# Kernel optimization log

Measured on AMD Instinct MI355X. Metric: run time of the kernel, lower is better.

Reference implementation:

```python
import jax, jax.numpy as jnp
import numpy as np

B, F_IN, N_D, N_A, VBS, N_STEPS = 1024, 256, 64, 64, 128, 3
FO = N_D + N_A            # 128
D_CAT = 2 * F_IN          # 512
AD = F_IN                 # attention_dim = 256
GAMMA, EPSILON, BN_EPS = 1.3, 1e-15, 1e-5
SQRT_HALF = 0.7071067811865476


def _bn(x, w, b):
    # full-batch BatchNorm1d (training mode, biased var)
    m = x.mean(0)
    v = x.var(0)
    return (x - m) / jnp.sqrt(v + BN_EPS) * w + b


def _gbn(x, w, b):
    # Ghost BatchNorm: per virtual-batch statistics
    n, f = x.shape
    xr = x.reshape(n // VBS, VBS, f)
    m = xr.mean(1, keepdims=True)
    v = xr.var(1, keepdims=True)
    return (xr - m).reshape(n, f) / jnp.sqrt(v + BN_EPS).repeat(VBS, axis=0).reshape(n, f) * w + b


def _glu(x, fcw, bnw, bnb):
    h = _gbn(x @ fcw.T, bnw, bnb)
    d = h.shape[-1] // 2
    return h[:, :d] * jax.nn.sigmoid(h[:, d:])


def _feat_transformer(x, fc0, bnw0, bnb0, fc1, bnw1, bnb1):
    # independent GLU block, first=True, n_glu_independent=2
    h = _glu(x, fc0, bnw0, bnb0)
    return (h + _glu(h, fc1, bnw1, bnb1)) * SQRT_HALF


def _sparsemax(z):
    f = z.shape[-1]
    zs = -jnp.sort(-z, axis=-1)                      # descending
    k = jnp.arange(1, f + 1, dtype=z.dtype)
    zc = jnp.cumsum(zs, axis=-1)
    support = (1.0 + k * zs) > zc
    kz = jnp.sum(support, axis=-1, keepdims=True)
    tau = (jnp.take_along_axis(zc, kz - 1, axis=-1) - 1.0) / kz.astype(z.dtype)
    return jnp.maximum(z - tau, 0.0)


def _self_attn_1d(x, in_w, in_b, out_w, out_b):
    # nn.MultiheadAttention(embed_dim=1, heads=1) over the feature axis
    q = x * in_w[0] + in_b[0]
    k = x * in_w[1] + in_b[1]
    v = x * in_w[2] + in_b[2]
    attn = jax.nn.softmax(jnp.einsum('bi,bj->bij', q, k), axis=-1)  # scale 1/sqrt(1)
    y = jnp.einsum('bij,bj->bi', attn, v) * out_w + out_b
    return y, attn


def setup_inputs() -> dict:
    key = jax.random.key(0)
    ks = iter(jax.random.split(key, 32))
    s = 0.1
    d = {
        'x': jax.random.normal(next(ks), (B, F_IN), jnp.float32),
        'bemv': jax.random.normal(next(ks), (B, F_IN), jnp.float32),
        'gmat': jax.random.uniform(next(ks), (AD, F_IN), jnp.float32),
        'bn_w': jnp.ones((F_IN,), jnp.float32),
        'bn_b': jnp.zeros((F_IN,), jnp.float32),
        'init_fc0': jax.random.normal(next(ks), (2 * FO, D_CAT), jnp.float32) * s,
        'init_bnw0': jnp.ones((2 * FO,), jnp.float32),
        'init_bnb0': jnp.zeros((2 * FO,), jnp.float32),
        'init_fc1': jax.random.normal(next(ks), (2 * FO, FO), jnp.float32) * s,
        'init_bnw1': jnp.ones((2 * FO,), jnp.float32),
        'init_bnb1': jnp.zeros((2 * FO,), jnp.float32),
        'step_fc0': jax.random.normal(next(ks), (N_STEPS, 2 * FO, D_CAT), jnp.float32) * s,
        'step_bnw0': jnp.ones((N_STEPS, 2 * FO), jnp.float32),
        'step_bnb0': jnp.zeros((N_STEPS, 2 * FO), jnp.float32),
        'step_fc1': jax.random.normal(next(ks), (N_STEPS, 2 * FO, FO), jnp.float32) * s,
        'step_bnw1': jnp.ones((N_STEPS, 2 * FO), jnp.float32),
        'step_bnb1': jnp.zeros((N_STEPS, 2 * FO), jnp.float32),
        'att_fc': jax.random.normal(next(ks), (N_STEPS, AD, N_A), jnp.float32) * s,
        'att_bnw': jnp.ones((N_STEPS, AD), jnp.float32),
        'att_bnb': jnp.zeros((N_STEPS, AD), jnp.float32),
        'sa_in_w': jax.random.normal(next(ks), (N_STEPS, 3), jnp.float32),
        'sa_in_b': jnp.zeros((N_STEPS, 3), jnp.float32),
        'sa_out_w': jax.random.normal(next(ks), (N_STEPS,), jnp.float32),
        'sa_out_b': jnp.zeros((N_STEPS,), jnp.float32),
    }
    return d


def reference(x, bemv, gmat, bn_w, bn_b,
              init_fc0, init_bnw0, init_bnb0, init_fc1, init_bnw1, init_bnb1,
              step_fc0, step_bnw0, step_bnb0, step_fc1, step_bnw1, step_bnb1,
              att_fc, att_bnw, att_bnb,
              sa_in_w, sa_in_b, sa_out_w, sa_out_b):
    prior = jnp.ones((x.shape[0], AD), x.dtype)
    xn = _bn(x, bn_w, bn_b)
    x_cat = jnp.concatenate([xn, bemv], axis=1)
    feat_out = _feat_transformer(x_cat, init_fc0, init_bnw0, init_bnb0,
                                 init_fc1, init_bnw1, init_bnb1)
    att = feat_out[:, N_D:]
    m_loss = jnp.asarray(0.0, x.dtype)
    steps, amaps = [], []
    for s in range(N_STEPS):
        a = _gbn(att @ att_fc[s].T, att_bnw[s], att_bnb[s])
        tab_mask = _sparsemax(a * prior)
        m_loss = m_loss + jnp.mean(jnp.sum(tab_mask * jnp.log(tab_mask + EPSILON), axis=1))
        prior = prior * (GAMMA - tab_mask)
        x_masked = (tab_mask @ gmat) * xn
        x_masked, A = _self_attn_1d(x_masked, sa_in_w[s], sa_in_b[s], sa_out_w[s], sa_out_b[s])
        amaps.append(A)
        feat_out = _feat_transformer(jnp.concatenate([x_masked, bemv], axis=1),
                                     step_fc0[s], step_bnw0[s], step_bnb0[s],
                                     step_fc1[s], step_bnw1[s], step_bnb1[s])
        steps.append(jax.nn.leaky_relu(feat_out[:, :N_D], 0.01))
        att = feat_out[:, N_D:]
    m_loss = m_loss / N_STEPS
    return jnp.stack(steps), m_loss, jnp.stack(amaps)
```

## Files before the change

kernel.cpp:

```cpp
#include <hip/hip_runtime.h>
#include <hip/hip_bf16.h>

#define BATCH 1024
#define F_IN 256
#define N_D 64
#define N_A 64
#define VBS 128
#define N_STEPS 3
#define FO 128
#define D_CAT 512
#define AD 256
#define GAMMA_C 1.3f
#define BN_EPS_C 1e-5f
#define SQRT_HALF_C 0.70710678118654752440f

__device__ __forceinline__ float ldin(const void* p, size_t i, int isbf){
  if (isbf) return __bfloat162float(((const __hip_bfloat16*)p)[i]);
  return ((const float*)p)[i];
}
__device__ __forceinline__ float4 ld4(const void* p, size_t i, int isbf){
  if (!isbf) return *(const float4*)((const float*)p + i);
  const __hip_bfloat16* q = (const __hip_bfloat16*)p + i;
  return make_float4(__bfloat162float(q[0]), __bfloat162float(q[1]),
                     __bfloat162float(q[2]), __bfloat162float(q[3]));
}

__device__ __forceinline__ float wsum(float v){
#pragma unroll
  for (int o = 32; o > 0; o >>= 1) v += __shfl_xor(v, o);
  return v;
}
__device__ __forceinline__ float wmaxr(float v){
#pragma unroll
  for (int o = 32; o > 0; o >>= 1) v = fmaxf(v, __shfl_xor(v, o));
  return v;
}
__device__ __forceinline__ float wminr(float v){
#pragma unroll
  for (int o = 32; o > 0; o >>= 1) v = fminf(v, __shfl_xor(v, o));
  return v;
}
__device__ __forceinline__ float block_sum(float v, float* sb){
  int t = threadIdx.x;
  sb[t] = v; __syncthreads();
#pragma unroll
  for (int s = 128; s > 0; s >>= 1){
    if (t < s) sb[t] += sb[t + s];
    __syncthreads();
  }
  float r = sb[0]; __syncthreads();
  return r;
}

__global__ void detect_k(const unsigned short* __restrict__ u, float* __restrict__ flag){
  __shared__ int cnt;
  if (threadIdx.x == 0) cnt = 0;
  __syncthreads();
  int c = 0;
  for (int j = 0; j < 16; ++j){
    unsigned short v = u[(size_t)(threadIdx.x * 16 + j) * 2];
    int e = (v >> 7) & 0xFF;
    if (e >= 118 && e <= 134) c++;
  }
  atomicAdd(&cnt, c);
  __syncthreads();
  if (threadIdx.x == 0) flag[0] = (cnt > 2048) ? 1.0f : 0.0f;
}

__global__ void bnstats_k(const void* __restrict__ x, float* __restrict__ mean,
                          float* __restrict__ istd, const float* __restrict__ flg){
  __shared__ float sb[256];
  const int isbf = flg[0] != 0.0f;
  int f = blockIdx.x, t = threadIdx.x;
  float s = 0.f, ss = 0.f;
  for (int r = t; r < BATCH; r += 256){
    float v = ldin(x, (size_t)r * F_IN + f, isbf);
    s += v; ss += v * v;
  }
  s  = block_sum(s, sb);
  ss = block_sum(ss, sb);
  if (t == 0){
    float m = s * (1.f / BATCH);
    mean[f] = m;
    istd[f] = rsqrtf(ss * (1.f / BATCH) - m * m + BN_EPS_C);
  }
}

__global__ void xn_k(const void* __restrict__ x, const float* __restrict__ mean,
                     const float* __restrict__ istd, const void* __restrict__ bw,
                     const void* __restrict__ bb, float* __restrict__ xn,
                     const float* __restrict__ flg){
  const int isbf = flg[0] != 0.0f;
  int idx = blockIdx.x * 256 + threadIdx.x;
  int f = idx & (F_IN - 1);
  xn[idx] = (ldin(x, idx, isbf) - mean[f]) * istd[f] * ldin(bw, f, isbf) + ldin(bb, f, isbf);
}

__global__ __launch_bounds__(256)
void gemm_bt_k(const float* __restrict__ A1, const void* __restrict__ A2, int split,
               const void* __restrict__ W, size_t woff, float* __restrict__ C,
               int K, const float* __restrict__ flg){
  __shared__ float As[32][34];
  __shared__ float Ws[32][34];
  const int isbf = flg[0] != 0.0f;
  const int n0 = blockIdx.x * 32, m0 = blockIdx.y * 32;
  const int t = threadIdx.x;
  const int tx = t & 15, ty = t >> 4;
  const int lr = t >> 3, lk = (t & 7) * 4;
  const int nc = K >> 5;
  float a00 = 0.f, a01 = 0.f, a10 = 0.f, a11 = 0.f;

  auto lda = [&](int k0) -> float4 {
    int gk = k0 + lk, gr = m0 + lr;
    if (gk < split) return *(const float4*)(A1 + (size_t)gr * split + gk);
    return ld4(A2, (size_t)gr * (K - split) + (gk - split), isbf);
  };
  auto ldw = [&](int k0) -> float4 {
    return ld4(W, woff + (size_t)(n0 + lr) * K + k0 + lk, isbf);
  };

  float4 ra = lda(0), rw = ldw(0);
  for (int c = 0; c < nc; ++c){
    As[lk+0][lr] = ra.x; As[lk+1][lr] = ra.y; As[lk+2][lr] = ra.z; As[lk+3][lr] = ra.w;
    Ws[lk+0][lr] = rw.x; Ws[lk+1][lr] = rw.y; Ws[lk+2][lr] = rw.z; Ws[lk+3][lr] = rw.w;
    __syncthreads();
    float4 na = ra, nw = rw;
    if (c + 1 < nc){ na = lda((c+1) << 5); nw = ldw((c+1) << 5); }
#pragma unroll
    for (int kk = 0; kk < 32; ++kk){
      float2 av = *(const float2*)&As[kk][ty*2];
      float2 wv = *(const float2*)&Ws[kk][tx*2];
      a00 += av.x * wv.x; a01 += av.x * wv.y;
      a10 += av.y * wv.x; a11 += av.y * wv.y;
    }
    __syncthreads();
    ra = na; rw = nw;
  }
  int r0 = m0 + ty*2, c0 = n0 + tx*2;
  float* Cp = C + (size_t)r0 * 256 + c0;
  Cp[0] = a00; Cp[1] = a01; Cp[256] = a10; Cp[257] = a11;
}

__global__ __launch_bounds__(256)
void gemm_glu_k(const float* __restrict__ H1, const float* __restrict__ saf,
                const float* __restrict__ sbf, const void* __restrict__ W,
                size_t woff, float* __restrict__ C, const float* __restrict__ flg){
  __shared__ float As[32][34];
  __shared__ float Ws[32][34];
  const int isbf = flg[0] != 0.0f;
  const int n0 = blockIdx.x * 32, m0 = blockIdx.y * 32;
  const int t = threadIdx.x;
  const int tx = t & 15, ty = t >> 4;
  const int lr = t >> 3, lk = (t & 7) * 4;
  float a00 = 0.f, a01 = 0.f, a10 = 0.f, a11 = 0.f;

  auto lda = [&](int k0) -> float4 {
    int gk = k0 + lk, gr = m0 + lr, g = gr >> 7;
    float4 h0 = *(const float4*)(H1 + (size_t)gr*256 + gk);
    float4 h1 = *(const float4*)(H1 + (size_t)gr*256 + gk + 128);
    float4 A0 = *(const float4*)(saf + g*256 + gk);
    float4 B0 = *(const float4*)(sbf + g*256 + gk);
    float4 A1 = *(const float4*)(saf + g*256 + gk + 128);
    float4 B1 = *(const float4*)(sbf + g*256 + gk + 128);
    float4 r;
    r.x = (h0.x*A0.x + B0.x) / (1.f + __expf(-(h1.x*A1.x + B1.x)));
    r.y = (h0.y*A0.y + B0.y) / (1.f + __expf(-(h1.y*A1.y + B1.y)));
    r.z = (h0.z*A0.z + B0.z) / (1.f + __expf(-(h1.z*A1.z + B1.z)));
    r.w = (h0.w*A0.w + B0.w) / (1.f + __expf(-(h1.w*A1.w + B1.w)));
    return r;
  };
  auto ldw = [&](int k0) -> float4 {
    return ld4(W, woff + (size_t)(n0 + lr) * 128 + k0 + lk, isbf);
  };

  float4 ra = lda(0), rw = ldw(0);
#pragma unroll 1
  for (int c = 0; c < 4; ++c){
    As[lk+0][lr] = ra.x; As[lk+1][lr] = ra.y; As[lk+2][lr] = ra.z; As[lk+3][lr] = ra.w;
    Ws[lk+0][lr] = rw.x; Ws[lk+1][lr] = rw.y; Ws[lk+2][lr] = rw.z; Ws[lk+3][lr] = rw.w;
    __syncthreads();
    float4 na = ra, nw = rw;
    if (c + 1 < 4){ na = lda((c+1) << 5); nw = ldw((c+1) << 5); }
#pragma unroll
    for (int kk = 0; kk < 32; ++kk){
      float2 av = *(const float2*)&As[kk][ty*2];
      float2 wv = *(const float2*)&Ws[kk][tx*2];
      a00 += av.x * wv.x; a01 += av.x * wv.y;
      a10 += av.y * wv.x; a11 += av.y * wv.y;
    }
    __syncthreads();
    ra = na; rw = nw;
  }
  int r0 = m0 + ty*2, c0 = n0 + tx*2;
  float* Cp = C + (size_t)r0 * 256 + c0;
  Cp[0] = a00; Cp[1] = a01; Cp[256] = a10; Cp[257] = a11;
}

__global__ __launch_bounds__(256)
void gstats_k(const float* __restrict__ H, const void* __restrict__ w,
              const void* __restrict__ b, size_t off, float* __restrict__ sa,
              float* __restrict__ sb, const float* __restrict__ flg){
  __shared__ float ps[8][32], pss[8][32];
  const int isbf = flg[0] != 0.0f;
  int c0 = blockIdx.x * 32, g = blockIdx.y;
  int tx = threadIdx.x & 31, q = threadIdx.x >> 5;
  const float* Hp = H + ((size_t)g*128 + q*16) * 256 + c0 + tx;
  float s = 0.f, ss = 0.f;
#pragma unroll
  for (int i = 0; i < 16; ++i){ float v = Hp[(size_t)i*256]; s += v; ss += v*v; }
  ps[q][tx] = s; pss[q][tx] = ss;
  __syncthreads();
  if (threadIdx.x < 32){
    int t = threadIdx.x, col = c0 + t;
    float S = 0.f, SS = 0.f;
#pragma unroll
    for (int qq = 0; qq < 8; ++qq){ S += ps[qq][t]; SS += pss[qq][t]; }
    float m = S * (1.f/128), is = rsqrtf(SS * (1.f/128) - m*m + BN_EPS_C);
    float wv = ldin(w, off + col, isbf), bv = ldin(b, off + col, isbf);
    float A = is * wv;
    sa[g*256 + col] = A;
    sb[g*256 + col] = bv - m * A;
  }
}

__global__ __launch_bounds__(256)
void spmaxxm_k(const float* __restrict__ H, const float* __restrict__ sa,
               const float* __restrict__ sb, float* __restrict__ prior,
               const float* __restrict__ xn, const void* __restrict__ gmat,
               float* __restrict__ xm, float* __restrict__ lrow,
               int first, const float* __restrict__ flg){
  __shared__ __align__(16) float tabs[4][256];
  __shared__ unsigned int msk[4][2];
  const int isbf = flg[0] != 0.0f;
  int lane = threadIdx.x & 63, wv = threadIdx.x >> 6;
  int b0 = blockIdx.x * 4;
  int b = b0 + wv, g = b >> 7;
  size_t rb = (size_t)b * 256;
  int j0 = lane * 4;
  float4 h4 = *(const float4*)(H + rb + j0);
  float4 A4 = *(const float4*)(sa + (size_t)g*256 + j0);
  float4 B4 = *(const float4*)(sb + (size_t)g*256 + j0);
  float pr[4];
  if (first){ pr[0] = pr[1] = pr[2] = pr[3] = 1.f; }
  else { float4 p4 = *(const float4*)(prior + rb + j0); pr[0]=p4.x; pr[1]=p4.y; pr[2]=p4.z; pr[3]=p4.w; }
  float z[4];
  z[0] = (h4.x*A4.x + B4.x) * pr[0];
  z[1] = (h4.y*A4.y + B4.y) * pr[1];
  z[2] = (h4.z*A4.z + B4.z) * pr[2];
  z[3] = (h4.w*A4.w + B4.w) * pr[3];
  float zm = wmaxr(fmaxf(fmaxf(z[0], z[1]), fmaxf(z[2], z[3])));
  float lo = zm - 1.f, hi = zm;
#pragma unroll 1
  for (int it = 0; it < 30; ++it){
    float mid = 0.5f * (lo + hi);
    float s = 0.f;
#pragma unroll
    for (int e = 0; e < 4; ++e){ float d = z[e] - mid; s += d > 0.f ? d : 0.f; }
    s = wsum(s);
    if (s >= 1.f) lo = mid; else hi = mid;
  }
  float tau = 0.5f * (lo + hi);
  float p[4], ls = 0.f;
#pragma unroll
  for (int e = 0; e < 4; ++e){
    p[e] = z[e] - tau; p[e] = p[e] > 0.f ? p[e] : 0.f;
    ls += p[e] * __logf(p[e] + 1e-15f);
  }
  *(float4*)&tabs[wv][j0] = make_float4(p[0], p[1], p[2], p[3]);
  *(float4*)(prior + rb + j0) = make_float4(pr[0]*(GAMMA_C - p[0]), pr[1]*(GAMMA_C - p[1]),
                                            pr[2]*(GAMMA_C - p[2]), pr[3]*(GAMMA_C - p[3]));
  ls = wsum(ls);
  if (lane == 0) lrow[b] = ls;
  bool nz = (p[0] > 0.f) | (p[1] > 0.f) | (p[2] > 0.f) | (p[3] > 0.f);
  unsigned long long bm = __ballot(nz);
  if (lane == 0){ msk[wv][0] = (unsigned int)bm; msk[wv][1] = (unsigned int)(bm >> 32); }
  __syncthreads();
  int t = threadIdx.x;
  unsigned long long M0 = msk[0][0] | ((unsigned long long)msk[0][1] << 32);
  unsigned long long M1 = msk[1][0] | ((unsigned long long)msk[1][1] << 32);
  unsigned long long M2 = msk[2][0] | ((unsigned long long)msk[2][1] << 32);
  unsigned long long M3 = msk[3][0] | ((unsigned long long)msk[3][1] << 32);
  float a0 = 0.f, a1 = 0.f, a2 = 0.f, a3 = 0.f;
#pragma unroll 1
  for (int c = 0; c < 64; ++c){
    int r0a = (int)((M0 >> c) & 1), r1a = (int)((M1 >> c) & 1);
    int r2a = (int)((M2 >> c) & 1), r3a = (int)((M3 >> c) & 1);
    if (r0a | r1a | r2a | r3a){
      int k = c * 4;
      float g0 = ldin(gmat, (size_t)(k+0)*256 + t, isbf);
      float g1 = ldin(gmat, (size_t)(k+1)*256 + t, isbf);
      float g2 = ldin(gmat, (size_t)(k+2)*256 + t, isbf);
      float g3 = ldin(gmat, (size_t)(k+3)*256 + t, isbf);
      if (r0a){ float4 tv = *(float4*)&tabs[0][k]; a0 += tv.x*g0 + tv.y*g1 + tv.z*g2 + tv.w*g3; }
      if (r1a){ float4 tv = *(float4*)&tabs[1][k]; a1 += tv.x*g0 + tv.y*g1 + tv.z*g2 + tv.w*g3; }
      if (r2a){ float4 tv = *(float4*)&tabs[2][k]; a2 += tv.x*g0 + tv.y*g1 + tv.z*g2 + tv.w*g3; }
      if (r3a){ float4 tv = *(float4*)&tabs[3][k]; a3 += tv.x*g0 + tv.y*g1 + tv.z*g2 + tv.w*g3; }
    }
  }
  xm[(size_t)(b0+0)*256 + t] = a0 * xn[(size_t)(b0+0)*256 + t];
  xm[(size_t)(b0+1)*256 + t] = a1 * xn[(size_t)(b0+1)*256 + t];
  xm[(size_t)(b0+2)*256 + t] = a2 * xn[(size_t)(b0+2)*256 + t];
  xm[(size_t)(b0+3)*256 + t] = a3 * xn[(size_t)(b0+3)*256 + t];
}

__global__ __launch_bounds__(256)
void attn_k(const float* __restrict__ xm, float* __restrict__ y,
            const void* __restrict__ in_w, const void* __restrict__ in_b,
            const void* __restrict__ out_w, const void* __restrict__ out_b,
            int s, float* __restrict__ amap, const float* __restrict__ flg){
  __shared__ __align__(16) float qs[256], ks[256], vs[256], ms[256], rz[256];
  __shared__ float r1[4], r2[4];
  const int isbf = flg[0] != 0.0f;
  int b = blockIdx.x, t = threadIdx.x;
  float w0 = ldin(in_w, s*3+0, isbf), w1 = ldin(in_w, s*3+1, isbf), w2 = ldin(in_w, s*3+2, isbf);
  float b0 = ldin(in_b, s*3+0, isbf), b1 = ldin(in_b, s*3+1, isbf), b2 = ldin(in_b, s*3+2, isbf);
  float ow = ldin(out_w, s, isbf), ob = ldin(out_b, s, isbf);
  float xv = xm[(size_t)b*256 + t];
  float q = xv*w0 + b0, k = xv*w1 + b1, v = xv*w2 + b2;
  qs[t] = q; ks[t] = k; vs[t] = v;
  int lane = t & 63, wv = t >> 6;
  float km = wmaxr(k), kn = wminr(k);
  if (lane == 0){ r1[wv] = km; r2[wv] = kn; }
  __syncthreads();
  float kmax = fmaxf(fmaxf(r1[0], r1[1]), fmaxf(r1[2], r1[3]));
  float kmin = fminf(fminf(r2[0], r2[1]), fminf(r2[2], r2[3]));
  float mi = (q >= 0.f) ? q*kmax : q*kmin;
  float Z = 0.f, Y = 0.f;
#pragma unroll 8
  for (int j = 0; j < 256; j += 4){
    float4 k4 = *(const float4*)&ks[j];
    float4 v4 = *(const float4*)&vs[j];
    float e0 = __expf(q*k4.x - mi), e1 = __expf(q*k4.y - mi);
    float e2 = __expf(q*k4.z - mi), e3 = __expf(q*k4.w - mi);
    Z += (e0 + e1) + (e2 + e3);
    Y += (e0*v4.x + e1*v4.y) + (e2*v4.z + e3*v4.w);
  }
  float rzv = 1.f / Z;
  y[(size_t)b*256 + t] = Y*rzv*ow + ob;
  ms[t] = mi; rz[t] = rzv;
  __syncthreads();
  int c0 = (t & 127) * 2;
  int rh = (t >> 7) * 128;
  float k0 = ks[c0], k1 = ks[c0 + 1];
  size_t base = ((size_t)s*BATCH + b) * 65536 + c0;
#pragma unroll 8
  for (int i = 0; i < 128; i += 4){
    int r = rh + i;
    float4 q4 = *(const float4*)&qs[r];
    float4 m4 = *(const float4*)&ms[r];
    float4 s4 = *(const float4*)&rz[r];
    float e00 = __expf(q4.x*k0 - m4.x) * s4.x, e01 = __expf(q4.x*k1 - m4.x) * s4.x;
    float e10 = __expf(q4.y*k0 - m4.y) * s4.y, e11 = __expf(q4.y*k1 - m4.y) * s4.y;
    float e20 = __expf(q4.z*k0 - m4.z) * s4.z, e21 = __expf(q4.z*k1 - m4.z) * s4.z;
    float e30 = __expf(q4.w*k0 - m4.w) * s4.w, e31 = __expf(q4.w*k1 - m4.w) * s4.w;
    *(float2*)(amap + base + (size_t)(r+0)*256) = make_float2(e00, e01);
    *(float2*)(amap + base + (size_t)(r+1)*256) = make_float2(e10, e11);
    *(float2*)(amap + base + (size_t)(r+2)*256) = make_float2(e20, e21);
    *(float2*)(amap + base + (size_t)(r+3)*256) = make_float2(e30, e31);
  }
}

__global__ __launch_bounds__(256)
void combine_k(const float* __restrict__ H1, const float* __restrict__ sa0,
               const float* __restrict__ sb0, const float* __restrict__ H2,
               const float* __restrict__ sa1, const float* __restrict__ sb1,
               float* __restrict__ att, float* __restrict__ steps_out){
  int r = blockIdx.x * 2 + (threadIdx.x >> 7);
  int j = threadIdx.x & 127;
  int g = r >> 7;
  float h0 = H1[(size_t)r*256 + j],  h1 = H1[(size_t)r*256 + j + 128];
  float n0 = h0 * sa0[g*256 + j]     + sb0[g*256 + j];
  float n1 = h1 * sa0[g*256 + j+128] + sb0[g*256 + j+128];
  float g0 = n0 / (1.f + __expf(-n1));
  float h2 = H2[(size_t)r*256 + j],  h3 = H2[(size_t)r*256 + j + 128];
  float m0 = h2 * sa1[g*256 + j]     + sb1[g*256 + j];
  float m1 = h3 * sa1[g*256 + j+128] + sb1[g*256 + j+128];
  float g1 = m0 / (1.f + __expf(-m1));
  float f = (g0 + g1) * SQRT_HALF_C;
  if (j < 64){
    if (steps_out) steps_out[(size_t)r*64 + j] = f > 0.f ? f : 0.01f*f;
  } else {
    att[(size_t)r*64 + (j - 64)] = f;
  }
}

__global__ void mloss_k(const float* __restrict__ lrow, float* __restrict__ outp){
  __shared__ float sb[256];
  int t = threadIdx.x;
  float s = 0.f;
  for (int i = t; i < N_STEPS*BATCH; i += 256) s += lrow[i];
  s = block_sum(s, sb);
  if (t == 0) outp[0] = s * (1.f/(N_STEPS*(float)BATCH));
}

extern "C" void kernel_launch(void* const* d_in, const int* in_sizes, int n_in,
                              void* d_out, int out_size, void* d_ws, size_t ws_size,
                              hipStream_t stream){
  const void* x         = d_in[0];
  const void* bemv      = d_in[1];
  const void* gmat      = d_in[2];
  const void* bn_w      = d_in[3];
  const void* bn_b      = d_in[4];
  const void* init_fc0  = d_in[5];
  const void* init_bnw0 = d_in[6];
  const void* init_bnb0 = d_in[7];
  const void* init_fc1  = d_in[8];
  const void* init_bnw1 = d_in[9];
  const void* init_bnb1 = d_in[10];
  const void* step_fc0  = d_in[11];
  const void* step_bnw0 = d_in[12];
  const void* step_bnb0 = d_in[13];
  const void* step_fc1  = d_in[14];
  const void* step_bnw1 = d_in[15];
  const void* step_bnb1 = d_in[16];
  const void* att_fc    = d_in[17];
  const void* att_bnw   = d_in[18];
  const void* att_bnb   = d_in[19];
  const void* sa_in_w   = d_in[20];
  const void* sa_in_b   = d_in[21];
  const void* sa_out_w  = d_in[22];
  const void* sa_out_b  = d_in[23];

  float* out       = (float*)d_out;
  float* steps_out = out;
  float* mloss_out = out + (size_t)N_STEPS*BATCH*N_D;
  float* amaps     = mloss_out + 1;

  float* w     = (float*)d_ws;
  float* flag  = w;
  float* mean  = w + 16;
  float* istd  = w + 272;
  float* lrow  = w + 528;
  float* sa0   = w + 4096;
  float* sb0   = sa0 + 2048;
  float* sa1   = sb0 + 2048;
  float* sb1   = sa1 + 2048;
  float* saA   = sb1 + 2048;
  float* sbA   = saA + 2048;
  float* xn    = w + 16384;
  float* H1    = xn   + 262144;
  float* H2    = H1   + 262144;
  float* att   = H2   + 262144;
  float* xm    = att  + 65536;
  float* prior = xm   + 262144;
  float* y     = prior + 262144;

  dim3 gemmGrid(8, 32);
  dim3 gstGrid(8, 8);

  detect_k<<<1, 256, 0, stream>>>((const unsigned short*)x, flag);
  bnstats_k<<<256, 256, 0, stream>>>(x, mean, istd, flag);
  xn_k<<<1024, 256, 0, stream>>>(x, mean, istd, bn_w, bn_b, xn, flag);

  gemm_bt_k<<<gemmGrid, 256, 0, stream>>>(xn, bemv, 256, init_fc0, 0, H1, 512, flag);
  gstats_k<<<gstGrid, 256, 0, stream>>>(H1, init_bnw0, init_bnb0, 0, sa0, sb0, flag);
  gemm_glu_k<<<gemmGrid, 256, 0, stream>>>(H1, sa0, sb0, init_fc1, 0, H2, flag);
  gstats_k<<<gstGrid, 256, 0, stream>>>(H2, init_bnw1, init_bnb1, 0, sa1, sb1, flag);
  combine_k<<<512, 256, 0, stream>>>(H1, sa0, sb0, H2, sa1, sb1, att, nullptr);

  for (int s = 0; s < N_STEPS; ++s){
    gemm_bt_k<<<gemmGrid, 256, 0, stream>>>(att, nullptr, 64, att_fc, (size_t)s*AD*N_A, H1, 64, flag);
    gstats_k<<<gstGrid, 256, 0, stream>>>(H1, att_bnw, att_bnb, (size_t)s*256, saA, sbA, flag);
    spmaxxm_k<<<256, 256, 0, stream>>>(H1, saA, sbA, prior, xn, gmat, xm, lrow + s*1024, s == 0, flag);
    attn_k<<<1024, 256, 0, stream>>>(xm, y, sa_in_w, sa_in_b, sa_out_w, sa_out_b, s, amaps, flag);
    gemm_bt_k<<<gemmGrid, 256, 0, stream>>>(y, bemv, 256, step_fc0, (size_t)s*256*512, H1, 512, flag);
    gstats_k<<<gstGrid, 256, 0, stream>>>(H1, step_bnw0, step_bnb0, (size_t)s*256, sa0, sb0, flag);
    gemm_glu_k<<<gemmGrid, 256, 0, stream>>>(H1, sa0, sb0, step_fc1, (size_t)s*256*128, H2, flag);
    gstats_k<<<gstGrid, 256, 0, stream>>>(H2, step_bnw1, step_bnb1, (size_t)s*256, sa1, sb1, flag);
    combine_k<<<512, 256, 0, stream>>>(H1, sa0, sb0, H2, sa1, sb1, att,
                                       steps_out + (size_t)s*BATCH*N_D);
  }
  mloss_k<<<1, 256, 0, stream>>>(lrow, mloss_out);
}
```

Before: 440.4 us.

## Fuse whole TabNet forward into one persistent kernel with grid barriers

Replaces the roughly 30 separate kernel launches with a single persistent kernel of 256 blocks. The former kernels become stages separated by a software grid barrier built on global atomics, and the stages share one shared-memory union. The aim is to remove per-launch overhead and gaps between launches on this small, latency-bound workload. In exchange, every stage is limited to 256 blocks, some stages (gstats) leave most blocks idle, and the spin barrier assumes all 256 blocks are co-resident and costs atomic round trips at each sync.

```diff
diff --git a/kernel.cpp b/kernel.cpp
--- a/kernel.cpp
+++ b/kernel.cpp
@@ -2,17 +2,11 @@
 #include <hip/hip_bf16.h>
 
 #define BATCH 1024
-#define F_IN 256
-#define N_D 64
-#define N_A 64
-#define VBS 128
 #define N_STEPS 3
-#define FO 128
-#define D_CAT 512
-#define AD 256
 #define GAMMA_C 1.3f
 #define BN_EPS_C 1e-5f
 #define SQRT_HALF_C 0.70710678118654752440f
+#define NBLK 256
 
 __device__ __forceinline__ float ldin(const void* p, size_t i, int isbf){
   if (isbf) return __bfloat162float(((const __hip_bfloat16*)p)[i]);
@@ -40,6 +34,14 @@
   for (int o = 32; o > 0; o >>= 1) v = fminf(v, __shfl_xor(v, o));
   return v;
 }
+
+struct SmGemm { float As[32][34]; float Ws[32][34]; };
+struct SmAttn { float qs[256], ks[256], vs[256], ms[256], rz[256]; float r1[4], r2[4]; };
+struct SmSp   { float tabs[4][256]; unsigned int msk[4][2]; };
+struct SmGst  { float ps[8][32], pss[8][32]; };
+struct SmRed  { float sb[256]; };
+union Smem { SmGemm g; SmAttn a; SmSp s; SmGst t; SmRed r; };
+
 __device__ __forceinline__ float block_sum(float v, float* sb){
   int t = threadIdx.x;
   sb[t] = v; __syncthreads();
@@ -52,84 +54,40 @@
   return r;
 }
 
-__global__ void detect_k(const unsigned short* __restrict__ u, float* __restrict__ flag){
-  __shared__ int cnt;
-  if (threadIdx.x == 0) cnt = 0;
+__device__ __forceinline__ void gbar(unsigned* bar){
   __syncthreads();
-  int c = 0;
-  for (int j = 0; j < 16; ++j){
-    unsigned short v = u[(size_t)(threadIdx.x * 16 + j) * 2];
-    int e = (v >> 7) & 0xFF;
-    if (e >= 118 && e <= 134) c++;
-  }
-  atomicAdd(&cnt, c);
+  if (threadIdx.x == 0){
+    __threadfence();
+    unsigned g = atomicAdd(&bar[1], 0u);
+    if (atomicAdd(&bar[0], 1u) == NBLK - 1u){
+      atomicExch(&bar[0], 0u);
+      __threadfence();
+      atomicAdd(&bar[1], 1u);
+    } else {
+      while (atomicAdd(&bar[1], 0u) == g){ __builtin_amdgcn_s_sleep(2); }
+    }
+    __threadfence();
+  }
   __syncthreads();
-  if (threadIdx.x == 0) flag[0] = (cnt > 2048) ? 1.0f : 0.0f;
-}
-
-__global__ void bnstats_k(const void* __restrict__ x, float* __restrict__ mean,
-                          float* __restrict__ istd, const float* __restrict__ flg){
-  __shared__ float sb[256];
-  const int isbf = flg[0] != 0.0f;
-  int f = blockIdx.x, t = threadIdx.x;
-  float s = 0.f, ss = 0.f;
-  for (int r = t; r < BATCH; r += 256){
-    float v = ldin(x, (size_t)r * F_IN + f, isbf);
-    s += v; ss += v * v;
-  }
-  s  = block_sum(s, sb);
-  ss = block_sum(ss, sb);
-  if (t == 0){
-    float m = s * (1.f / BATCH);
-    mean[f] = m;
-    istd[f] = rsqrtf(ss * (1.f / BATCH) - m * m + BN_EPS_C);
-  }
-}
-
-__global__ void xn_k(const void* __restrict__ x, const float* __restrict__ mean,
-                     const float* __restrict__ istd, const void* __restrict__ bw,
-                     const void* __restrict__ bb, float* __restrict__ xn,
-                     const float* __restrict__ flg){
-  const int isbf = flg[0] != 0.0f;
-  int idx = blockIdx.x * 256 + threadIdx.x;
-  int f = idx & (F_IN - 1);
-  xn[idx] = (ldin(x, idx, isbf) - mean[f]) * istd[f] * ldin(bw, f, isbf) + ldin(bb, f, isbf);
-}
-
-__global__ __launch_bounds__(256)
-void gemm_bt_k(const float* __restrict__ A1, const void* __restrict__ A2, int split,
-               const void* __restrict__ W, size_t woff, float* __restrict__ C,
-               int K, const float* __restrict__ flg){
-  __shared__ float As[32][34];
-  __shared__ float Ws[32][34];
-  const int isbf = flg[0] != 0.0f;
-  const int n0 = blockIdx.x * 32, m0 = blockIdx.y * 32;
-  const int t = threadIdx.x;
+}
+
+template<typename FA, typename FW>
+__device__ __forceinline__ void gemm_body(FA&& lda, FW&& ldw, int nc, SmGemm& g,
+                                          int t, int n0, int m0, float* C){
   const int tx = t & 15, ty = t >> 4;
   const int lr = t >> 3, lk = (t & 7) * 4;
-  const int nc = K >> 5;
   float a00 = 0.f, a01 = 0.f, a10 = 0.f, a11 = 0.f;
-
-  auto lda = [&](int k0) -> float4 {
-    int gk = k0 + lk, gr = m0 + lr;
-    if (gk < split) return *(const float4*)(A1 + (size_t)gr * split + gk);
-    return ld4(A2, (size_t)gr * (K - split) + (gk - split), isbf);
-  };
-  auto ldw = [&](int k0) -> float4 {
-    return ld4(W, woff + (size_t)(n0 + lr) * K + k0 + lk, isbf);
-  };
-
-  float4 ra = lda(0), rw = ldw(0);
-  for (int c = 0; c < nc; ++c){
-    As[lk+0][lr] = ra.x; As[lk+1][lr] = ra.y; As[lk+2][lr] = ra.z; As[lk+3][lr] = ra.w;
-    Ws[lk+0][lr] = rw.x; Ws[lk+1][lr] = rw.y; Ws[lk+2][lr] = rw.z; Ws[lk+3][lr] = rw.w;
+  float4 ra = lda(0, lr, lk), rw = ldw(0, lr, lk);
+  for (int c2 = 0; c2 < nc; ++c2){
+    g.As[lk+0][lr] = ra.x; g.As[lk+1][lr] = ra.y; g.As[lk+2][lr] = ra.z; g.As[lk+3][lr] = ra.w;
+    g.Ws[lk+0][lr] = rw.x; g.Ws[lk+1][lr] = rw.y; g.Ws[lk+2][lr] = rw.z; g.Ws[lk+3][lr] = rw.w;
     __syncthreads();
     float4 na = ra, nw = rw;
-    if (c + 1 < nc){ na = lda((c+1) << 5); nw = ldw((c+1) << 5); }
+    if (c2 + 1 < nc){ na = lda((c2+1) << 5, lr, lk); nw = ldw((c2+1) << 5, lr, lk); }
 #pragma unroll
     for (int kk = 0; kk < 32; ++kk){
-      float2 av = *(const float2*)&As[kk][ty*2];
-      float2 wv = *(const float2*)&Ws[kk][tx*2];
+      float2 av = *(const float2*)&g.As[kk][ty*2];
+      float2 wv = *(const float2*)&g.Ws[kk][tx*2];
       a00 += av.x * wv.x; a01 += av.x * wv.y;
       a10 += av.y * wv.x; a11 += av.y * wv.y;
     }
@@ -141,334 +99,417 @@
   Cp[0] = a00; Cp[1] = a01; Cp[256] = a10; Cp[257] = a11;
 }
 
-__global__ __launch_bounds__(256)
-void gemm_glu_k(const float* __restrict__ H1, const float* __restrict__ saf,
-                const float* __restrict__ sbf, const void* __restrict__ W,
-                size_t woff, float* __restrict__ C, const float* __restrict__ flg){
-  __shared__ float As[32][34];
-  __shared__ float Ws[32][34];
-  const int isbf = flg[0] != 0.0f;
-  const int n0 = blockIdx.x * 32, m0 = blockIdx.y * 32;
-  const int t = threadIdx.x;
-  const int tx = t & 15, ty = t >> 4;
-  const int lr = t >> 3, lk = (t & 7) * 4;
-  float a00 = 0.f, a01 = 0.f, a10 = 0.f, a11 = 0.f;
-
-  auto lda = [&](int k0) -> float4 {
-    int gk = k0 + lk, gr = m0 + lr, g = gr >> 7;
-    float4 h0 = *(const float4*)(H1 + (size_t)gr*256 + gk);
-    float4 h1 = *(const float4*)(H1 + (size_t)gr*256 + gk + 128);
-    float4 A0 = *(const float4*)(saf + g*256 + gk);
-    float4 B0 = *(const float4*)(sbf + g*256 + gk);
-    float4 A1 = *(const float4*)(saf + g*256 + gk + 128);
-    float4 B1 = *(const float4*)(sbf + g*256 + gk + 128);
-    float4 r;
-    r.x = (h0.x*A0.x + B0.x) / (1.f + __expf(-(h1.x*A1.x + B1.x)));
-    r.y = (h0.y*A0.y + B0.y) / (1.f + __expf(-(h1.y*A1.y + B1.y)));
-    r.z = (h0.z*A0.z + B0.z) / (1.f + __expf(-(h1.z*A1.z + B1.z)));
-    r.w = (h0.w*A0.w + B0.w) / (1.f + __expf(-(h1.w*A1.w + B1.w)));
-    return r;
-  };
-  auto ldw = [&](int k0) -> float4 {
-    return ld4(W, woff + (size_t)(n0 + lr) * 128 + k0 + lk, isbf);
-  };
-
-  float4 ra = lda(0), rw = ldw(0);
-#pragma unroll 1
-  for (int c = 0; c < 4; ++c){
-    As[lk+0][lr] = ra.x; As[lk+1][lr] = ra.y; As[lk+2][lr] = ra.z; As[lk+3][lr] = ra.w;
-    Ws[lk+0][lr] = rw.x; Ws[lk+1][lr] = rw.y; Ws[lk+2][lr] = rw.z; Ws[lk+3][lr] = rw.w;
-    __syncthreads();
-    float4 na = ra, nw = rw;
-    if (c + 1 < 4){ na = lda((c+1) << 5); nw = ldw((c+1) << 5); }
-#pragma unroll
-    for (int kk = 0; kk < 32; ++kk){
-      float2 av = *(const float2*)&As[kk][ty*2];
-      float2 wv = *(const float2*)&Ws[kk][tx*2];
-      a00 += av.x * wv.x; a01 += av.x * wv.y;
-      a10 += av.y * wv.x; a11 += av.y * wv.y;
-    }
-    __syncthreads();
-    ra = na; rw = nw;
-  }
-  int r0 = m0 + ty*2, c0 = n0 + tx*2;
-  float* Cp = C + (size_t)r0 * 256 + c0;
-  Cp[0] = a00; Cp[1] = a01; Cp[256] = a10; Cp[257] = a11;
-}
-
-__global__ __launch_bounds__(256)
-void gstats_k(const float* __restrict__ H, const void* __restrict__ w,
-              const void* __restrict__ b, size_t off, float* __restrict__ sa,
-              float* __restrict__ sb, const float* __restrict__ flg){
-  __shared__ float ps[8][32], pss[8][32];
-  const int isbf = flg[0] != 0.0f;
-  int c0 = blockIdx.x * 32, g = blockIdx.y;
-  int tx = threadIdx.x & 31, q = threadIdx.x >> 5;
+__device__ __forceinline__ void gstats_body(SmGst& G, const float* H, const void* w,
+    const void* b, size_t off, float* sa, float* sb, int isbf, int bid, int t){
+  int c0 = (bid & 7) * 32, g = bid >> 3;
+  int tx = t & 31, q = t >> 5;
   const float* Hp = H + ((size_t)g*128 + q*16) * 256 + c0 + tx;
   float s = 0.f, ss = 0.f;
 #pragma unroll
   for (int i = 0; i < 16; ++i){ float v = Hp[(size_t)i*256]; s += v; ss += v*v; }
-  ps[q][tx] = s; pss[q][tx] = ss;
+  G.ps[q][tx] = s; G.pss[q][tx] = ss;
   __syncthreads();
-  if (threadIdx.x < 32){
-    int t = threadIdx.x, col = c0 + t;
+  if (t < 32){
+    int col = c0 + t;
     float S = 0.f, SS = 0.f;
 #pragma unroll
-    for (int qq = 0; qq < 8; ++qq){ S += ps[qq][t]; SS += pss[qq][t]; }
+    for (int qq = 0; qq < 8; ++qq){ S += G.ps[qq][t]; SS += G.pss[qq][t]; }
     float m = S * (1.f/128), is = rsqrtf(SS * (1.f/128) - m*m + BN_EPS_C);
     float wv = ldin(w, off + col, isbf), bv = ldin(b, off + col, isbf);
     float A = is * wv;
     sa[g*256 + col] = A;
     sb[g*256 + col] = bv - m * A;
   }
+  __syncthreads();
+}
+
+__device__ __forceinline__ float combine_scalar(const float* H1, const float* H2,
+    const float* sa0, const float* sb0, const float* sa1, const float* sb1, int r, int j){
+  int g = r >> 7;
+  float h0 = H1[(size_t)r*256 + j], h1 = H1[(size_t)r*256 + j + 128];
+  float u0 = h0 * sa0[g*256 + j]     + sb0[g*256 + j];
+  float u1 = h1 * sa0[g*256 + j+128] + sb0[g*256 + j+128];
+  float g0 = u0 / (1.f + __expf(-u1));
+  float v0 = H2[(size_t)r*256 + j]     * sa1[g*256 + j]     + sb1[g*256 + j];
+  float v1 = H2[(size_t)r*256 + j+128] * sa1[g*256 + j+128] + sb1[g*256 + j+128];
+  float g1 = v0 / (1.f + __expf(-v1));
+  return (g0 + g1) * SQRT_HALF_C;
+}
+
+struct KParams {
+  const void *x, *bemv, *gmat, *bn_w, *bn_b;
+  const void *ifc0, *ibnw0, *ibnb0, *ifc1, *ibnw1, *ibnb1;
+  const void *sfc0, *sbnw0, *sbnb0, *sfc1, *sbnw1, *sbnb1;
+  const void *afc, *abnw, *abnb;
+  const void *siw, *sib, *sow, *sob;
+  float* out; float* ws;
+};
+
+__global__ void initbar_k(float* ws){
+  unsigned* bar = (unsigned*)(ws + 3584);
+  bar[0] = 0u; bar[1] = 0u;
 }
 
 __global__ __launch_bounds__(256)
-void spmaxxm_k(const float* __restrict__ H, const float* __restrict__ sa,
-               const float* __restrict__ sb, float* __restrict__ prior,
-               const float* __restrict__ xn, const void* __restrict__ gmat,
-               float* __restrict__ xm, float* __restrict__ lrow,
-               int first, const float* __restrict__ flg){
-  __shared__ __align__(16) float tabs[4][256];
-  __shared__ unsigned int msk[4][2];
-  const int isbf = flg[0] != 0.0f;
-  int lane = threadIdx.x & 63, wv = threadIdx.x >> 6;
-  int b0 = blockIdx.x * 4;
-  int b = b0 + wv, g = b >> 7;
-  size_t rb = (size_t)b * 256;
-  int j0 = lane * 4;
-  float4 h4 = *(const float4*)(H + rb + j0);
-  float4 A4 = *(const float4*)(sa + (size_t)g*256 + j0);
-  float4 B4 = *(const float4*)(sb + (size_t)g*256 + j0);
-  float pr[4];
-  if (first){ pr[0] = pr[1] = pr[2] = pr[3] = 1.f; }
-  else { float4 p4 = *(const float4*)(prior + rb + j0); pr[0]=p4.x; pr[1]=p4.y; pr[2]=p4.z; pr[3]=p4.w; }
-  float z[4];
-  z[0] = (h4.x*A4.x + B4.x) * pr[0];
-  z[1] = (h4.y*A4.y + B4.y) * pr[1];
-  z[2] = (h4.z*A4.z + B4.z) * pr[2];
-  z[3] = (h4.w*A4.w + B4.w) * pr[3];
-  float zm = wmaxr(fmaxf(fmaxf(z[0], z[1]), fmaxf(z[2], z[3])));
-  float lo = zm - 1.f, hi = zm;
-#pragma unroll 1
-  for (int it = 0; it < 30; ++it){
-    float mid = 0.5f * (lo + hi);
-    float s = 0.f;
-#pragma unroll
-    for (int e = 0; e < 4; ++e){ float d = z[e] - mid; s += d > 0.f ? d : 0.f; }
-    s = wsum(s);
-    if (s >= 1.f) lo = mid; else hi = mid;
-  }
-  float tau = 0.5f * (lo + hi);
-  float p[4], ls = 0.f;
-#pragma unroll
-  for (int e = 0; e < 4; ++e){
-    p[e] = z[e] - tau; p[e] = p[e] > 0.f ? p[e] : 0.f;
-    ls += p[e] * __logf(p[e] + 1e-15f);
-  }
-  *(float4*)&tabs[wv][j0] = make_float4(p[0], p[1], p[2], p[3]);
-  *(float4*)(prior + rb + j0) = make_float4(pr[0]*(GAMMA_C - p[0]), pr[1]*(GAMMA_C - p[1]),
-                                            pr[2]*(GAMMA_C - p[2]), pr[3]*(GAMMA_C - p[3]));
-  ls = wsum(ls);
-  if (lane == 0) lrow[b] = ls;
-  bool nz = (p[0] > 0.f) | (p[1] > 0.f) | (p[2] > 0.f) | (p[3] > 0.f);
-  unsigned long long bm = __ballot(nz);
-  if (lane == 0){ msk[wv][0] = (unsigned int)bm; msk[wv][1] = (unsigned int)(bm >> 32); }
-  __syncthreads();
-  int t = threadIdx.x;
-  unsigned long long M0 = msk[0][0] | ((unsigned long long)msk[0][1] << 32);
-  unsigned long long M1 = msk[1][0] | ((unsigned long long)msk[1][1] << 32);
-  unsigned long long M2 = msk[2][0] | ((unsigned long long)msk[2][1] << 32);
-  unsigned long long M3 = msk[3][0] | ((unsigned long long)msk[3][1] << 32);
-  float a0 = 0.f, a1 = 0.f, a2 = 0.f, a3 = 0.f;
-#pragma unroll 1
-  for (int c = 0; c < 64; ++c){
-    int r0a = (int)((M0 >> c) & 1), r1a = (int)((M1 >> c) & 1);
-    int r2a = (int)((M2 >> c) & 1), r3a = (int)((M3 >> c) & 1);
-    if (r0a | r1a | r2a | r3a){
-      int k = c * 4;
-      float g0 = ldin(gmat, (size_t)(k+0)*256 + t, isbf);
-      float g1 = ldin(gmat, (size_t)(k+1)*256 + t, isbf);
-      float g2 = ldin(gmat, (size_t)(k+2)*256 + t, isbf);
-      float g3 = ldin(gmat, (size_t)(k+3)*256 + t, isbf);
-      if (r0a){ float4 tv = *(float4*)&tabs[0][k]; a0 += tv.x*g0 + tv.y*g1 + tv.z*g2 + tv.w*g3; }
-      if (r1a){ float4 tv = *(float4*)&tabs[1][k]; a1 += tv.x*g0 + tv.y*g1 + tv.z*g2 + tv.w*g3; }
-      if (r2a){ float4 tv = *(float4*)&tabs[2][k]; a2 += tv.x*g0 + tv.y*g1 + tv.z*g2 + tv.w*g3; }
-      if (r3a){ float4 tv = *(float4*)&tabs[3][k]; a3 += tv.x*g0 + tv.y*g1 + tv.z*g2 + tv.w*g3; }
-    }
-  }
-  xm[(size_t)(b0+0)*256 + t] = a0 * xn[(size_t)(b0+0)*256 + t];
-  xm[(size_t)(b0+1)*256 + t] = a1 * xn[(size_t)(b0+1)*256 + t];
-  xm[(size_t)(b0+2)*256 + t] = a2 * xn[(size_t)(b0+2)*256 + t];
-  xm[(size_t)(b0+3)*256 + t] = a3 * xn[(size_t)(b0+3)*256 + t];
-}
-
-__global__ __launch_bounds__(256)
-void attn_k(const float* __restrict__ xm, float* __restrict__ y,
-            const void* __restrict__ in_w, const void* __restrict__ in_b,
-            const void* __restrict__ out_w, const void* __restrict__ out_b,
-            int s, float* __restrict__ amap, const float* __restrict__ flg){
-  __shared__ __align__(16) float qs[256], ks[256], vs[256], ms[256], rz[256];
-  __shared__ float r1[4], r2[4];
-  const int isbf = flg[0] != 0.0f;
-  int b = blockIdx.x, t = threadIdx.x;
-  float w0 = ldin(in_w, s*3+0, isbf), w1 = ldin(in_w, s*3+1, isbf), w2 = ldin(in_w, s*3+2, isbf);
-  float b0 = ldin(in_b, s*3+0, isbf), b1 = ldin(in_b, s*3+1, isbf), b2 = ldin(in_b, s*3+2, isbf);
-  float ow = ldin(out_w, s, isbf), ob = ldin(out_b, s, isbf);
-  float xv = xm[(size_t)b*256 + t];
-  float q = xv*w0 + b0, k = xv*w1 + b1, v = xv*w2 + b2;
-  qs[t] = q; ks[t] = k; vs[t] = v;
-  int lane = t & 63, wv = t >> 6;
-  float km = wmaxr(k), kn = wminr(k);
-  if (lane == 0){ r1[wv] = km; r2[wv] = kn; }
-  __syncthreads();
-  float kmax = fmaxf(fmaxf(r1[0], r1[1]), fmaxf(r1[2], r1[3]));
-  float kmin = fminf(fminf(r2[0], r2[1]), fminf(r2[2], r2[3]));
-  float mi = (q >= 0.f) ? q*kmax : q*kmin;
-  float Z = 0.f, Y = 0.f;
-#pragma unroll 8
-  for (int j = 0; j < 256; j += 4){
-    float4 k4 = *(const float4*)&ks[j];
-    float4 v4 = *(const float4*)&vs[j];
-    float e0 = __expf(q*k4.x - mi), e1 = __expf(q*k4.y - mi);
-    float e2 = __expf(q*k4.z - mi), e3 = __expf(q*k4.w - mi);
-    Z += (e0 + e1) + (e2 + e3);
-    Y += (e0*v4.x + e1*v4.y) + (e2*v4.z + e3*v4.w);
-  }
-  float rzv = 1.f / Z;
-  y[(size_t)b*256 + t] = Y*rzv*ow + ob;
-  ms[t] = mi; rz[t] = rzv;
-  __syncthreads();
-  int c0 = (t & 127) * 2;
-  int rh = (t >> 7) * 128;
-  float k0 = ks[c0], k1 = ks[c0 + 1];
-  size_t base = ((size_t)s*BATCH + b) * 65536 + c0;
-#pragma unroll 8
-  for (int i = 0; i < 128; i += 4){
-    int r = rh + i;
-    float4 q4 = *(const float4*)&qs[r];
-    float4 m4 = *(const float4*)&ms[r];
-    float4 s4 = *(const float4*)&rz[r];
-    float e00 = __expf(q4.x*k0 - m4.x) * s4.x, e01 = __expf(q4.x*k1 - m4.x) * s4.x;
-    float e10 = __expf(q4.y*k0 - m4.y) * s4.y, e11 = __expf(q4.y*k1 - m4.y) * s4.y;
-    float e20 = __expf(q4.z*k0 - m4.z) * s4.z, e21 = __expf(q4.z*k1 - m4.z) * s4.z;
-    float e30 = __expf(q4.w*k0 - m4.w) * s4.w, e31 = __expf(q4.w*k1 - m4.w) * s4.w;
-    *(float2*)(amap + base + (size_t)(r+0)*256) = make_float2(e00, e01);
-    *(float2*)(amap + base + (size_t)(r+1)*256) = make_float2(e10, e11);
-    *(float2*)(amap + base + (size_t)(r+2)*256) = make_float2(e20, e21);
-    *(float2*)(amap + base + (size_t)(r+3)*256) = make_float2(e30, e31);
-  }
-}
-
-__global__ __launch_bounds__(256)
-void combine_k(const float* __restrict__ H1, const float* __restrict__ sa0,
-               const float* __restrict__ sb0, const float* __restrict__ H2,
-               const float* __restrict__ sa1, const float* __restrict__ sb1,
-               float* __restrict__ att, float* __restrict__ steps_out){
-  int r = blockIdx.x * 2 + (threadIdx.x >> 7);
-  int j = threadIdx.x & 127;
-  int g = r >> 7;
-  float h0 = H1[(size_t)r*256 + j],  h1 = H1[(size_t)r*256 + j + 128];
-  float n0 = h0 * sa0[g*256 + j]     + sb0[g*256 + j];
-  float n1 = h1 * sa0[g*256 + j+128] + sb0[g*256 + j+128];
-  float g0 = n0 / (1.f + __expf(-n1));
-  float h2 = H2[(size_t)r*256 + j],  h3 = H2[(size_t)r*256 + j + 128];
-  float m0 = h2 * sa1[g*256 + j]     + sb1[g*256 + j];
-  float m1 = h3 * sa1[g*256 + j+128] + sb1[g*256 + j+128];
-  float g1 = m0 / (1.f + __expf(-m1));
-  float f = (g0 + g1) * SQRT_HALF_C;
-  if (j < 64){
-    if (steps_out) steps_out[(size_t)r*64 + j] = f > 0.f ? f : 0.01f*f;
-  } else {
-    att[(size_t)r*64 + (j - 64)] = f;
-  }
-}
-
-__global__ void mloss_k(const float* __restrict__ lrow, float* __restrict__ outp){
-  __shared__ float sb[256];
-  int t = threadIdx.x;
-  float s = 0.f;
-  for (int i = t; i < N_STEPS*BATCH; i += 256) s += lrow[i];
-  s = block_sum(s, sb);
-  if (t == 0) outp[0] = s * (1.f/(N_STEPS*(float)BATCH));
-}
-
-extern "C" void kernel_launch(void* const* d_in, const int* in_sizes, int n_in,
-                              void* d_out, int out_size, void* d_ws, size_t ws_size,
-                              hipStream_t stream){
-  const void* x         = d_in[0];
-  const void* bemv      = d_in[1];
-  const void* gmat      = d_in[2];
-  const void* bn_w      = d_in[3];
-  const void* bn_b      = d_in[4];
-  const void* init_fc0  = d_in[5];
-  const void* init_bnw0 = d_in[6];
-  const void* init_bnb0 = d_in[7];
-  const void* init_fc1  = d_in[8];
-  const void* init_bnw1 = d_in[9];
-  const void* init_bnb1 = d_in[10];
-  const void* step_fc0  = d_in[11];
-  const void* step_bnw0 = d_in[12];
-  const void* step_bnb0 = d_in[13];
-  const void* step_fc1  = d_in[14];
-  const void* step_bnw1 = d_in[15];
-  const void* step_bnb1 = d_in[16];
-  const void* att_fc    = d_in[17];
-  const void* att_bnw   = d_in[18];
-  const void* att_bnb   = d_in[19];
-  const void* sa_in_w   = d_in[20];
-  const void* sa_in_b   = d_in[21];
-  const void* sa_out_w  = d_in[22];
-  const void* sa_out_b  = d_in[23];
-
-  float* out       = (float*)d_out;
-  float* steps_out = out;
-  float* mloss_out = out + (size_t)N_STEPS*BATCH*N_D;
-  float* amaps     = mloss_out + 1;
-
-  float* w     = (float*)d_ws;
-  float* flag  = w;
-  float* mean  = w + 16;
-  float* istd  = w + 272;
-  float* lrow  = w + 528;
-  float* sa0   = w + 4096;
+void mega_k(KParams P){
+  const int bid = blockIdx.x, t = threadIdx.x;
+  __shared__ Smem sm;
+
+  float* ws    = P.ws;
+  float* xnA   = ws;
+  float* xnB   = ws + 256;
+  float* lrow  = ws + 512;
+  unsigned* bar = (unsigned*)(ws + 3584);
+  float* sa0   = ws + 4096;
   float* sb0   = sa0 + 2048;
   float* sa1   = sb0 + 2048;
   float* sb1   = sa1 + 2048;
   float* saA   = sb1 + 2048;
   float* sbA   = saA + 2048;
-  float* xn    = w + 16384;
+  float* xn    = ws + 16384;
   float* H1    = xn   + 262144;
   float* H2    = H1   + 262144;
-  float* att   = H2   + 262144;
-  float* xm    = att  + 65536;
+  float* Ha    = H2   + 262144;
+  float* xm    = Ha   + 262144;
   float* prior = xm   + 262144;
   float* y     = prior + 262144;
-
-  dim3 gemmGrid(8, 32);
-  dim3 gstGrid(8, 8);
-
-  detect_k<<<1, 256, 0, stream>>>((const unsigned short*)x, flag);
-  bnstats_k<<<256, 256, 0, stream>>>(x, mean, istd, flag);
-  xn_k<<<1024, 256, 0, stream>>>(x, mean, istd, bn_w, bn_b, xn, flag);
-
-  gemm_bt_k<<<gemmGrid, 256, 0, stream>>>(xn, bemv, 256, init_fc0, 0, H1, 512, flag);
-  gstats_k<<<gstGrid, 256, 0, stream>>>(H1, init_bnw0, init_bnb0, 0, sa0, sb0, flag);
-  gemm_glu_k<<<gemmGrid, 256, 0, stream>>>(H1, sa0, sb0, init_fc1, 0, H2, flag);
-  gstats_k<<<gstGrid, 256, 0, stream>>>(H2, init_bnw1, init_bnb1, 0, sa1, sb1, flag);
-  combine_k<<<512, 256, 0, stream>>>(H1, sa0, sb0, H2, sa1, sb1, att, nullptr);
+  float* amaps = P.out + 196609;
+
+  {
+    int c = 0;
+    const unsigned short* u = (const unsigned short*)P.x;
+    for (int j = 0; j < 16; ++j){
+      unsigned short v = u[(size_t)(t * 16 + j) * 2];
+      int e = (v >> 7) & 0xFF;
+      c += (e >= 118 && e <= 134);
+    }
+    float cf = block_sum((float)c, sm.r.sb);
+    sm.r.sb[0] = cf; __syncthreads();
+  }
+  const int isbf = sm.r.sb[0] > 2048.f;
+  __syncthreads();
+
+  {
+    int f = bid;
+    float s = 0.f, ss = 0.f;
+    for (int r = t; r < BATCH; r += 256){
+      float v = ldin(P.x, (size_t)r*256 + f, isbf);
+      s += v; ss += v*v;
+    }
+    s  = block_sum(s, sm.r.sb);
+    ss = block_sum(ss, sm.r.sb);
+    if (t == 0){
+      float m = s * (1.f/BATCH);
+      float is = rsqrtf(ss * (1.f/BATCH) - m*m + BN_EPS_C);
+      float A = is * ldin(P.bn_w, f, isbf);
+      xnA[f] = A;
+      xnB[f] = ldin(P.bn_b, f, isbf) - m * A;
+    }
+  }
+  gbar(bar);
+
+  {
+    const int n0 = (bid & 7) * 32, m0 = (bid >> 3) * 32;
+    auto lda = [&](int k0, int lr, int lk) -> float4 {
+      int gk = k0 + lk, gr = m0 + lr;
+      if (gk < 256){
+        float4 xv = ld4(P.x, (size_t)gr*256 + gk, isbf);
+        float4 A4 = *(const float4*)(xnA + gk);
+        float4 B4 = *(const float4*)(xnB + gk);
+        return make_float4(xv.x*A4.x+B4.x, xv.y*A4.y+B4.y, xv.z*A4.z+B4.z, xv.w*A4.w+B4.w);
+      }
+      return ld4(P.bemv, (size_t)gr*256 + (gk - 256), isbf);
+    };
+    auto ldw = [&](int k0, int lr, int lk) -> float4 {
+      return ld4(P.ifc0, (size_t)(n0 + lr)*512 + k0 + lk, isbf);
+    };
+    gemm_body(lda, ldw, 16, sm.g, t, n0, m0, H1);
+    int fi = (bid * 256 + t) * 4;
+    int col = fi & 255;
+    float4 xv = ld4(P.x, fi, isbf);
+    float4 A4 = *(const float4*)(xnA + col);
+    float4 B4 = *(const float4*)(xnB + col);
+    *(float4*)(xn + fi) = make_float4(xv.x*A4.x+B4.x, xv.y*A4.y+B4.y, xv.z*A4.z+B4.z, xv.w*A4.w+B4.w);
+  }
+  gbar(bar);
+
+  if (bid < 64) gstats_body(sm.t, H1, P.ibnw0, P.ibnb0, 0, sa0, sb0, isbf, bid, t);
+  gbar(bar);
+
+  {
+    const int n0 = (bid & 7) * 32, m0 = (bid >> 3) * 32;
+    auto lda = [&](int k0, int lr, int lk) -> float4 {
+      int gk = k0 + lk, gr = m0 + lr, g = gr >> 7;
+      const float* h = H1 + (size_t)gr*256;
+      float4 h0 = *(const float4*)(h + gk);
+      float4 h1 = *(const float4*)(h + gk + 128);
+      float4 A0 = *(const float4*)(sa0 + g*256 + gk);
+      float4 B0 = *(const float4*)(sb0 + g*256 + gk);
+      float4 A1 = *(const float4*)(sa0 + g*256 + gk + 128);
+      float4 B1 = *(const float4*)(sb0 + g*256 + gk + 128);
+      float4 r;
+      r.x = (h0.x*A0.x+B0.x) / (1.f + __expf(-(h1.x*A1.x+B1.x)));
+      r.y = (h0.y*A0.y+B0.y) / (1.f + __expf(-(h1.y*A1.y+B1.y)));
+      r.z = (h0.z*A0.z+B0.z) / (1.f + __expf(-(h1.z*A1.z+B1.z)));
+      r.w = (h0.w*A0.w+B0.w) / (1.f + __expf(-(h1.w*A1.w+B1.w)));
+      return r;
+    };
+    auto ldw = [&](int k0, int lr, int lk) -> float4 {
+      return ld4(P.ifc1, (size_t)(n0 + lr)*128 + k0 + lk, isbf);
+    };
+    gemm_body(lda, ldw, 4, sm.g, t, n0, m0, H2);
+  }
+  gbar(bar);
+
+  if (bid < 64) gstats_body(sm.t, H2, P.ibnw1, P.ibnb1, 0, sa1, sb1, isbf, bid, t);
+  gbar(bar);
 
   for (int s = 0; s < N_STEPS; ++s){
-    gemm_bt_k<<<gemmGrid, 256, 0, stream>>>(att, nullptr, 64, att_fc, (size_t)s*AD*N_A, H1, 64, flag);
-    gstats_k<<<gstGrid, 256, 0, stream>>>(H1, att_bnw, att_bnb, (size_t)s*256, saA, sbA, flag);
-    spmaxxm_k<<<256, 256, 0, stream>>>(H1, saA, sbA, prior, xn, gmat, xm, lrow + s*1024, s == 0, flag);
-    attn_k<<<1024, 256, 0, stream>>>(xm, y, sa_in_w, sa_in_b, sa_out_w, sa_out_b, s, amaps, flag);
-    gemm_bt_k<<<gemmGrid, 256, 0, stream>>>(y, bemv, 256, step_fc0, (size_t)s*256*512, H1, 512, flag);
-    gstats_k<<<gstGrid, 256, 0, stream>>>(H1, step_bnw0, step_bnb0, (size_t)s*256, sa0, sb0, flag);
-    gemm_glu_k<<<gemmGrid, 256, 0, stream>>>(H1, sa0, sb0, step_fc1, (size_t)s*256*128, H2, flag);
-    gstats_k<<<gstGrid, 256, 0, stream>>>(H2, step_bnw1, step_bnb1, (size_t)s*256, sa1, sb1, flag);
-    combine_k<<<512, 256, 0, stream>>>(H1, sa0, sb0, H2, sa1, sb1, att,
-                                       steps_out + (size_t)s*BATCH*N_D);
-  }
-  mloss_k<<<1, 256, 0, stream>>>(lrow, mloss_out);
-}
+    {
+      const int n0 = (bid & 7) * 32, m0 = (bid >> 3) * 32;
+      auto lda = [&](int k0, int lr, int lk) -> float4 {
+        int gk = k0 + lk, gr = m0 + lr, g = gr >> 7;
+        const float* h1p = H1 + (size_t)gr*256;
+        const float* h2p = H2 + (size_t)gr*256;
+        float4 a0 = *(const float4*)(h1p + gk + 64);
+        float4 a1 = *(const float4*)(h1p + gk + 192);
+        float4 c0 = *(const float4*)(sa0 + g*256 + gk + 64);
+        float4 d0 = *(const float4*)(sb0 + g*256 + gk + 64);
+        float4 c1 = *(const float4*)(sa0 + g*256 + gk + 192);
+        float4 d1 = *(const float4*)(sb0 + g*256 + gk + 192);
+        float4 b0 = *(const float4*)(h2p + gk + 64);
+        float4 b1 = *(const float4*)(h2p + gk + 192);
+        float4 e0 = *(const float4*)(sa1 + g*256 + gk + 64);
+        float4 f0 = *(const float4*)(sb1 + g*256 + gk + 64);
+        float4 e1 = *(const float4*)(sa1 + g*256 + gk + 192);
+        float4 f1 = *(const float4*)(sb1 + g*256 + gk + 192);
+        float4 r;
+        r.x = ((a0.x*c0.x+d0.x)/(1.f+__expf(-(a1.x*c1.x+d1.x)))
+             + (b0.x*e0.x+f0.x)/(1.f+__expf(-(b1.x*e1.x+f1.x)))) * SQRT_HALF_C;
+        r.y = ((a0.y*c0.y+d0.y)/(1.f+__expf(-(a1.y*c1.y+d1.y)))
+             + (b0.y*e0.y+f0.y)/(1.f+__expf(-(b1.y*e1.y+f1.y)))) * SQRT_HALF_C;
+        r.z = ((a0.z*c0.z+d0.z)/(1.f+__expf(-(a1.z*c1.z+d1.z)))
+             + (b0.z*e0.z+f0.z)/(1.f+__expf(-(b1.z*e1.z+f1.z)))) * SQRT_HALF_C;
+        r.w = ((a0.w*c0.w+d0.w)/(1.f+__expf(-(a1.w*c1.w+d1.w)))
+             + (b0.w*e0.w+f0.w)/(1.f+__expf(-(b1.w*e1.w+f1.w)))) * SQRT_HALF_C;
+        return r;
+      };
+      auto ldw = [&](int k0, int lr, int lk) -> float4 {
+        return ld4(P.afc, (size_t)s*16384 + (size_t)(n0 + lr)*64 + k0 + lk, isbf);
+      };
+      gemm_body(lda, ldw, 2, sm.g, t, n0, m0, Ha);
+      if (s > 0){
+        int idx = bid * 256 + t;
+        int r = idx >> 6, j = idx & 63;
+        float f = combine_scalar(H1, H2, sa0, sb0, sa1, sb1, r, j);
+        P.out[(size_t)(s-1)*65536 + idx] = f > 0.f ? f : 0.01f*f;
+      }
+    }
+    gbar(bar);
+
+    if (bid < 64) gstats_body(sm.t, Ha, P.abnw, P.abnb, (size_t)s*256, saA, sbA, isbf, bid, t);
+    gbar(bar);
+
+    {
+      int lane = t & 63, wv = t >> 6;
+      int b0 = bid * 4;
+      int b = b0 + wv, g = b >> 7;
+      size_t rb = (size_t)b * 256;
+      int j0 = lane * 4;
+      float4 h4 = *(const float4*)(Ha + rb + j0);
+      float4 A4 = *(const float4*)(saA + (size_t)g*256 + j0);
+      float4 B4 = *(const float4*)(sbA + (size_t)g*256 + j0);
+      float pr[4];
+      if (s == 0){ pr[0] = pr[1] = pr[2] = pr[3] = 1.f; }
+      else { float4 p4 = *(const float4*)(prior + rb + j0); pr[0]=p4.x; pr[1]=p4.y; pr[2]=p4.z; pr[3]=p4.w; }
+      float z[4];
+      z[0] = (h4.x*A4.x + B4.x) * pr[0];
+      z[1] = (h4.y*A4.y + B4.y) * pr[1];
+      z[2] = (h4.z*A4.z + B4.z) * pr[2];
+      z[3] = (h4.w*A4.w + B4.w) * pr[3];
+      float zm = wmaxr(fmaxf(fmaxf(z[0], z[1]), fmaxf(z[2], z[3])));
+      float lo = zm - 1.f, hi = zm;
+#pragma unroll 1
+      for (int it = 0; it < 30; ++it){
+        float mid = 0.5f * (lo + hi);
+        float sv = 0.f;
+#pragma unroll
+        for (int e = 0; e < 4; ++e){ float d = z[e] - mid; sv += d > 0.f ? d : 0.f; }
+        sv = wsum(sv);
+        if (sv >= 1.f) lo = mid; else hi = mid;
+      }
+      float tau = 0.5f * (lo + hi);
+      float p[4], ls = 0.f;
+#pragma unroll
+      for (int e = 0; e < 4; ++e){
+        p[e] = z[e] - tau; p[e] = p[e] > 0.f ? p[e] : 0.f;
+        ls += p[e] * __logf(p[e] + 1e-15f);
+      }
+      *(float4*)&sm.s.tabs[wv][j0] = make_float4(p[0], p[1], p[2], p[3]);
+      *(float4*)(prior + rb + j0) = make_float4(pr[0]*(GAMMA_C-p[0]), pr[1]*(GAMMA_C-p[1]),
+                                                pr[2]*(GAMMA_C-p[2]), pr[3]*(GAMMA_C-p[3]));
+      ls = wsum(ls);
+      if (lane == 0) lrow[s*1024 + b] = ls;
+      bool nz = (p[0] > 0.f) | (p[1] > 0.f) | (p[2] > 0.f) | (p[3] > 0.f);
+      unsigned long long bm = __ballot(nz);
+      if (lane == 0){ sm.s.msk[wv][0] = (unsigned int)bm; sm.s.msk[wv][1] = (unsigned int)(bm >> 32); }
+      __syncthreads();
+      unsigned long long M0 = sm.s.msk[0][0] | ((unsigned long long)sm.s.msk[0][1] << 32);
+      unsigned long long M1 = sm.s.msk[1][0] | ((unsigned long long)sm.s.msk[1][1] << 32);
+      unsigned long long M2 = sm.s.msk[2][0] | ((unsigned long long)sm.s.msk[2][1] << 32);
+      unsigned long long M3 = sm.s.msk[3][0] | ((unsigned long long)sm.s.msk[3][1] << 32);
+      float a0 = 0.f, a1 = 0.f, a2 = 0.f, a3 = 0.f;
+#pragma unroll 1
+      for (int c = 0; c < 64; ++c){
+        int r0a = (int)((M0 >> c) & 1), r1a = (int)((M1 >> c) & 1);
+        int r2a = (int)((M2 >> c) & 1), r3a = (int)((M3 >> c) & 1);
+        if (r0a | r1a | r2a | r3a){
+          int k = c * 4;
+          float g0 = ldin(P.gmat, (size_t)(k+0)*256 + t, isbf);
+          float g1 = ldin(P.gmat, (size_t)(k+1)*256 + t, isbf);
+          float g2 = ldin(P.gmat, (size_t)(k+2)*256 + t, isbf);
+          float g3 = ldin(P.gmat, (size_t)(k+3)*256 + t, isbf);
+          if (r0a){ float4 tv = *(float4*)&sm.s.tabs[0][k]; a0 += tv.x*g0 + tv.y*g1 + tv.z*g2 + tv.w*g3; }
+          if (r1a){ float4 tv = *(float4*)&sm.s.tabs[1][k]; a1 += tv.x*g0 + tv.y*g1 + tv.z*g2 + tv.w*g3; }
+          if (r2a){ float4 tv = *(float4*)&sm.s.tabs[2][k]; a2 += tv.x*g0 + tv.y*g1 + tv.z*g2 + tv.w*g3; }
+          if (r3a){ float4 tv = *(float4*)&sm.s.tabs[3][k]; a3 += tv.x*g0 + tv.y*g1 + tv.z*g2 + tv.w*g3; }
+        }
+      }
+      xm[(size_t)(b0+0)*256 + t] = a0 * xn[(size_t)(b0+0)*256 + t];
+      xm[(size_t)(b0+1)*256 + t] = a1 * xn[(size_t)(b0+1)*256 + t];
+      xm[(size_t)(b0+2)*256 + t] = a2 * xn[(size_t)(b0+2)*256 + t];
+      xm[(size_t)(b0+3)*256 + t] = a3 * xn[(size_t)(b0+3)*256 + t];
+    }
+    gbar(bar);
+
+    {
+      float w0 = ldin(P.siw, s*3+0, isbf), w1 = ldin(P.siw, s*3+1, isbf), w2 = ldin(P.siw, s*3+2, isbf);
+      float b0 = ldin(P.sib, s*3+0, isbf), b1 = ldin(P.sib, s*3+1, isbf), b2 = ldin(P.sib, s*3+2, isbf);
+      float ow = ldin(P.sow, s, isbf), ob = ldin(P.sob, s, isbf);
+      for (int it = 0; it < 4; ++it){
+        int b = it * 256 + bid;
+        float xv = xm[(size_t)b*256 + t];
+        float q = xv*w0 + b0, k = xv*w1 + b1, v = xv*w2 + b2;
+        sm.a.qs[t] = q; sm.a.ks[t] = k; sm.a.vs[t] = v;
+        int lane = t & 63, wv = t >> 6;
+        float km = wmaxr(k), kn = wminr(k);
+        if (lane == 0){ sm.a.r1[wv] = km; sm.a.r2[wv] = kn; }
+        __syncthreads();
+        float kmax = fmaxf(fmaxf(sm.a.r1[0], sm.a.r1[1]), fmaxf(sm.a.r1[2], sm.a.r1[3]));
+        float kmin = fminf(fminf(sm.a.r2[0], sm.a.r2[1]), fminf(sm.a.r2[2], sm.a.r2[3]));
+        float mi = (q >= 0.f) ? q*kmax : q*kmin;
+        float Z = 0.f, Y = 0.f;
+#pragma unroll 8
+        for (int j = 0; j < 256; j += 4){
+          float4 k4 = *(const float4*)&sm.a.ks[j];
+          float4 v4 = *(const float4*)&sm.a.vs[j];
+          float e0 = __expf(q*k4.x - mi), e1 = __expf(q*k4.y - mi);
+          float e2 = __expf(q*k4.z - mi), e3 = __expf(q*k4.w - mi);
+          Z += (e0 + e1) + (e2 + e3);
+          Y += (e0*v4.x + e1*v4.y) + (e2*v4.z + e3*v4.w);
+        }
+        float rzv = 1.f / Z;
+        y[(size_t)b*256 + t] = Y*rzv*ow + ob;
+        sm.a.ms[t] = mi; sm.a.rz[t] = rzv;
+        __syncthreads();
+        int c0 = (t & 127) * 2;
+        int rh = (t >> 7) * 128;
+        float k0 = sm.a.ks[c0], k1 = sm.a.ks[c0 + 1];
+        size_t base = ((size_t)s*BATCH + b) * 65536 + c0;
+#pragma unroll 8
+        for (int i = 0; i < 128; i += 4){
+          int r = rh + i;
+          float4 q4 = *(const float4*)&sm.a.qs[r];
+          float4 m4 = *(const float4*)&sm.a.ms[r];
+          float4 s4 = *(const float4*)&sm.a.rz[r];
+          float e00 = __expf(q4.x*k0 - m4.x) * s4.x, e01 = __expf(q4.x*k1 - m4.x) * s4.x;
+          float e10 = __expf(q4.y*k0 - m4.y) * s4.y, e11 = __expf(q4.y*k1 - m4.y) * s4.y;
+          float e20 = __expf(q4.z*k0 - m4.z) * s4.z, e21 = __expf(q4.z*k1 - m4.z) * s4.z;
+          float e30 = __expf(q4.w*k0 - m4.w) * s4.w, e31 = __expf(q4.w*k1 - m4.w) * s4.w;
+          *(float2*)(amaps + base + (size_t)(r+0)*256) = make_float2(e00, e01);
+          *(float2*)(amaps + base + (size_t)(r+1)*256) = make_float2(e10, e11);
+          *(float2*)(amaps + base + (size_t)(r+2)*256) = make_float2(e20, e21);
+          *(float2*)(amaps + base + (size_t)(r+3)*256) = make_float2(e30, e31);
+        }
+        __syncthreads();
+      }
+    }
+    gbar(bar);
+
+    {
+      const int n0 = (bid & 7) * 32, m0 = (bid >> 3) * 32;
+      auto lda = [&](int k0, int lr, int lk) -> float4 {
+        int gk = k0 + lk, gr = m0 + lr;
+        if (gk < 256) return *(const float4*)(y + (size_t)gr*256 + gk);
+        return ld4(P.bemv, (size_t)gr*256 + (gk - 256), isbf);
+      };
+      auto ldw = [&](int k0, int lr, int lk) -> float4 {
+        return ld4(P.sfc0, (size_t)s*131072 + (size_t)(n0 + lr)*512 + k0 + lk, isbf);
+      };
+      gemm_body(lda, ldw, 16, sm.g, t, n0, m0, H1);
+    }
+    gbar(bar);
+
+    if (bid < 64) gstats_body(sm.t, H1, P.sbnw0, P.sbnb0, (size_t)s*256, sa0, sb0, isbf, bid, t);
+    gbar(bar);
+
+    {
+      const int n0 = (bid & 7) * 32, m0 = (bid >> 3) * 32;
+      auto lda = [&](int k0, int lr, int lk) -> float4 {
+        int gk = k0 + lk, gr = m0 + lr, g = gr >> 7;
+        const float* h = H1 + (size_t)gr*256;
+        float4 h0 = *(const float4*)(h + gk);
+        float4 h1 = *(const float4*)(h + gk + 128);
+        float4 A0 = *(const float4*)(sa0 + g*256 + gk);
+        float4 B0 = *(const float4*)(sb0 + g*256 + gk);
+        float4 A1 = *(const float4*)(sa0 + g*256 + gk + 128);
+        float4 B1 = *(const float4*)(sb0 + g*256 + gk + 128);
+        float4 r;
+        r.x = (h0.x*A0.x+B0.x) / (1.f + __expf(-(h1.x*A1.x+B1.x)));
+        r.y = (h0.y*A0.y+B0.y) / (1.f + __expf(-(h1.y*A1.y+B1.y)));
+        r.z = (h0.z*A0.z+B0.z) / (1.f + __expf(-(h1.z*A1.z+B1.z)));
+        r.w = (h0.w*A0.w+B0.w) / (1.f + __expf(-(h1.w*A1.w+B1.w)));
+        return r;
+      };
+      auto ldw = [&](int k0, int lr, int lk) -> float4 {
+        return ld4(P.sfc1, (size_t)s*32768 + (size_t)(n0 + lr)*128 + k0 + lk, isbf);
+      };
+      gemm_body(lda, ldw, 4, sm.g, t, n0, m0, H2);
+    }
+    gbar(bar);
+
+    if (bid < 64) gstats_body(sm.t, H2, P.sbnw1, P.sbnb1, (size_t)s*256, sa1, sb1, isbf, bid, t);
+    gbar(bar);
+  }
+
+  {
+    int idx = bid * 256 + t;
+    int r = idx >> 6, j = idx & 63;
+    float f = combine_scalar(H1, H2, sa0, sb0, sa1, sb1, r, j);
+    P.out[(size_t)2*65536 + idx] = f > 0.f ? f : 0.01f*f;
+  }
+  if (bid == 0){
+    float ssum = 0.f;
+    for (int i = t; i < N_STEPS*BATCH; i += 256) ssum += lrow[i];
+    ssum = block_sum(ssum, sm.r.sb);
+    if (t == 0) P.out[196608] = ssum * (1.f/(N_STEPS*(float)BATCH));
+  }
+}
+
+extern "C" void kernel_launch(void* const* d_in, const int* in_sizes, int n_in,
+                              void* d_out, int out_size, void* d_ws, size_t ws_size,
+                              hipStream_t stream){
+  KParams P;
+  P.x     = d_in[0];  P.bemv  = d_in[1];  P.gmat  = d_in[2];
+  P.bn_w  = d_in[3];  P.bn_b  = d_in[4];
+  P.ifc0  = d_in[5];  P.ibnw0 = d_in[6];  P.ibnb0 = d_in[7];
+  P.ifc1  = d_in[8];  P.ibnw1 = d_in[9];  P.ibnb1 = d_in[10];
+  P.sfc0  = d_in[11]; P.sbnw0 = d_in[12]; P.sbnb0 = d_in[13];
+  P.sfc1  = d_in[14]; P.sbnw1 = d_in[15]; P.sbnb1 = d_in[16];
+  P.afc   = d_in[17]; P.abnw  = d_in[18]; P.abnb  = d_in[19];
+  P.siw   = d_in[20]; P.sib   = d_in[21]; P.sow   = d_in[22]; P.sob = d_in[23];
+  P.out   = (float*)d_out;
+  P.ws    = (float*)d_ws;
+  initbar_k<<<1, 1, 0, stream>>>(P.ws);
+  mega_k<<<NBLK, 256, 0, stream>>>(P);
+}
```

After: 1.123 ms. +155.1%, slower.
